# Optimization experiments

Measured on AMD Instinct MI355X. Metric: run time of the kernel, lower is better.

## Reference

```python
import jax, jax.numpy as jnp
import numpy as np

DIM = 1024
HID = 2732  # int(2*4*1024/3) rounded up to multiple of 4
E = 8
TOPK = 2
B, S = 2, 2048


def setup_inputs() -> dict:
    key = jax.random.key(0)
    ks = jax.random.split(key, 5)
    scale = 0.02
    return {
        "x": jax.random.normal(ks[0], (B, S, DIM), dtype=jnp.float32),
        "Wg": jax.random.normal(ks[1], (E, DIM), dtype=jnp.float32) * scale,
        "W1": jax.random.normal(ks[2], (E, HID, DIM), dtype=jnp.float32) * scale,
        "W2": jax.random.normal(ks[3], (E, DIM, HID), dtype=jnp.float32) * scale,
        "W3": jax.random.normal(ks[4], (E, HID, DIM), dtype=jnp.float32) * scale,
    }


def reference(x, Wg, W1, W2, W3):
    b, s, d = x.shape
    xt = x.reshape(b * s, d)                              # [N, d]
    scores = xt @ Wg.T                                    # [N, E]
    w, idx = jax.lax.top_k(scores, TOPK)                  # [N, k]
    w = jax.nn.softmax(w, axis=-1)
    n = xt.shape[0]
    # combine weights scattered back into [N, E] (top-k indices are distinct per row)
    cw = jnp.zeros((n, E), dtype=x.dtype).at[jnp.arange(n)[:, None], idx].set(w)
    # dense per-expert SwiGLU (mathematically identical to masked dispatch)
    h1 = jnp.einsum('nd,ehd->neh', xt, W1)                # [N, E, H]
    h3 = jnp.einsum('nd,ehd->neh', xt, W3)
    h = jax.nn.silu(h1) * h3
    y = jnp.einsum('neh,edh->ned', h, W2)                 # [N, E, d]
    out = jnp.einsum('ned,ne->nd', y, cw)                 # [N, d]
    return out
```

## Files before the change

### kernel.cpp

```cpp
#include <hip/hip_runtime.h>
#include <hip/hip_bf16.h>
#include <stdint.h>

#define DIM   1024
#define HID   2732
#define HPAD  2816
#define NEXP  8
#define NTOK  4096
#define NROW  8192
#define C13BLK 22528

typedef __attribute__((ext_vector_type(8))) short bf16x8;
typedef __attribute__((ext_vector_type(4))) float f32x4;

__device__ __forceinline__ unsigned short f2bf(float f) {
    union { float f; uint32_t u; } v; v.f = f;
    uint32_t u = v.u;
    return (unsigned short)((u + 0x7FFFu + ((u >> 16) & 1u)) >> 16);
}
__device__ __forceinline__ float bf2f(unsigned short h) {
    union { uint32_t u; float f; } v; v.u = ((uint32_t)h) << 16;
    return v.f;
}

#define ASYNC_CP16(g, l) __builtin_amdgcn_global_load_lds( \
    (const __attribute__((address_space(1))) void*)(g), \
    (__attribute__((address_space(3))) void*)(l), 16, 0, 0)

__device__ __forceinline__ void conv13_body(const float* __restrict__ src,
                                            unsigned short* __restrict__ dst, int blk) {
    size_t t = (size_t)blk * 256 + threadIdx.x;
    int d4 = (int)(t & 255);
    size_t rest = t >> 8;
    int hp = (int)(rest % HPAD);
    int e  = (int)(rest / HPAD);
    ushort4 o;
    if (hp < HID) {
        float4 v = *(const float4*)(src + ((size_t)e * HID + hp) * DIM + d4 * 4);
        o.x = f2bf(v.x); o.y = f2bf(v.y); o.z = f2bf(v.z); o.w = f2bf(v.w);
    } else {
        o.x = o.y = o.z = o.w = 0;
    }
    *(ushort4*)(dst + t * 4) = o;
}

__global__ void prep_kernel(const float* __restrict__ x,  const float* __restrict__ Wg,
                            const float* __restrict__ W1, const float* __restrict__ W2,
                            const float* __restrict__ W3,
                            unsigned short* __restrict__ W1b,
                            unsigned short* __restrict__ W2b,
                            unsigned short* __restrict__ W3b,
                            int* __restrict__ counts, int* __restrict__ a_exp,
                            int* __restrict__ a_rank, float* __restrict__ a_w) {
    int b = blockIdx.x;
    if (b < C13BLK) { conv13_body(W1, W1b, b); return; }
    b -= C13BLK;
    if (b < C13BLK) { conv13_body(W3, W3b, b); return; }
    b -= C13BLK;
    if (b < C13BLK) {
        size_t t = (size_t)b * 256 + threadIdx.x;
        int h4 = (int)(t % (HPAD / 4));
        size_t rest = t / (HPAD / 4);
        int d = (int)(rest % DIM);
        int e = (int)(rest / DIM);
        ushort4 o;
        if (h4 * 4 < HID) {
            float4 v = *(const float4*)(W2 + ((size_t)e * DIM + d) * HID + h4 * 4);
            o.x = f2bf(v.x); o.y = f2bf(v.y); o.z = f2bf(v.z); o.w = f2bf(v.w);
        } else {
            o.x = o.y = o.z = o.w = 0;
        }
        *(ushort4*)(W2b + t * 4) = o;
        return;
    }
    b -= C13BLK;
    int wave = threadIdx.x >> 6, lane = threadIdx.x & 63;
    int n = b * 4 + wave;
    const float* xr = x + (size_t)n * DIM + lane * 16;
    float p[NEXP];
#pragma unroll
    for (int e = 0; e < NEXP; ++e) p[e] = 0.f;
#pragma unroll
    for (int i = 0; i < 4; ++i) {
        float4 xv = *(const float4*)(xr + i * 4);
#pragma unroll
        for (int e = 0; e < NEXP; ++e) {
            float4 wv = *(const float4*)(Wg + e * DIM + lane * 16 + i * 4);
            p[e] += xv.x * wv.x + xv.y * wv.y + xv.z * wv.z + xv.w * wv.w;
        }
    }
#pragma unroll
    for (int off = 32; off > 0; off >>= 1)
#pragma unroll
        for (int e = 0; e < NEXP; ++e) p[e] += __shfl_xor(p[e], off);
    if (lane == 0) {
        int i1 = -1, i2 = -1; float m1 = -1e30f, m2 = -1e30f;
#pragma unroll
        for (int e = 0; e < NEXP; ++e) {
            float s = p[e];
            if (s > m1) { m2 = m1; i2 = i1; m1 = s; i1 = e; }
            else if (s > m2) { m2 = s; i2 = e; }
        }
        float e2 = __expf(m2 - m1);
        float inv = 1.f / (1.f + e2);
        int a = n * 2;
        a_exp[a] = i1;  a_w[a] = inv;        a_rank[a] = atomicAdd(&counts[i1], 1);
        a_exp[a+1] = i2; a_w[a+1] = e2 * inv; a_rank[a+1] = atomicAdd(&counts[i2], 1);
    }
}

__global__ void gather_kernel(const float* __restrict__ x, const int* __restrict__ a_exp,
                              const int* __restrict__ a_rank,
                              const int* __restrict__ counts,
                              unsigned short* __restrict__ XG,
                              int* __restrict__ row_of_a) {
    __shared__ int soff[NEXP];
    if (threadIdx.x == 0) {
        int s = 0;
#pragma unroll
        for (int e = 0; e < NEXP; ++e) { soff[e] = s; s += counts[e]; }
    }
    __syncthreads();
    int a = blockIdx.x, n = a >> 1;
    int row = soff[a_exp[a]] + a_rank[a];
    if (threadIdx.x == 0) row_of_a[a] = row;
    float4 xv = *(const float4*)(x + (size_t)n * DIM + threadIdx.x * 4);
    ushort4 o; o.x = f2bf(xv.x); o.y = f2bf(xv.y); o.z = f2bf(xv.z); o.w = f2bf(xv.w);
    *(ushort4*)(XG + (size_t)row * DIM + threadIdx.x * 4) = o;
}

__global__ __launch_bounds__(256, 2) void gemm1_kernel(
    const unsigned short* __restrict__ XG,
    const unsigned short* __restrict__ W1b,
    const unsigned short* __restrict__ W3b,
    const int* __restrict__ counts,
    unsigned short* __restrict__ Hbuf)
{
    const int e = blockIdx.z, mtile = blockIdx.y, ntile = blockIdx.x;
    const int cnt = counts[e];
    if (mtile * 128 >= cnt) return;
    int rowstart = 0;
    for (int i = 0; i < e; ++i) rowstart += counts[i];
    rowstart += mtile * 128;

    __shared__ __align__(16) unsigned short As[128 * 64];
    __shared__ __align__(16) unsigned short B1s[64 * 64];
    __shared__ __align__(16) unsigned short B3s[64 * 64];

    const int tid = threadIdx.x, lane = tid & 63, wave = tid >> 6;
    const int wm = wave >> 1, wn = wave & 1;
    const int quad = lane >> 4;

    const unsigned short* w1e = W1b + (size_t)e * HPAD * DIM;
    const unsigned short* w3e = W3b + (size_t)e * HPAD * DIM;

    const int srow = tid >> 3;
    const int scol = (((tid & 7) ^ (srow & 7)) * 8);
    const unsigned short* ag[4];
#pragma unroll
    for (int r = 0; r < 4; ++r) {
        int grow = rowstart + r * 32 + srow;
        if (grow > NROW - 1) grow = NROW - 1;
        ag[r] = XG + (size_t)grow * DIM + scol;
    }
    const unsigned short* bg1[2]; const unsigned short* bg3[2];
#pragma unroll
    for (int r = 0; r < 2; ++r) {
        int grow = ntile * 64 + r * 32 + srow;
        bg1[r] = w1e + (size_t)grow * DIM + scol;
        bg3[r] = w3e + (size_t)grow * DIM + scol;
    }

    f32x4 acc1[4][2], acc3[4][2];
#pragma unroll
    for (int i = 0; i < 4; ++i)
#pragma unroll
        for (int j = 0; j < 2; ++j) {
            acc1[i][j] = (f32x4){0.f, 0.f, 0.f, 0.f};
            acc3[i][j] = (f32x4){0.f, 0.f, 0.f, 0.f};
        }

    for (int kk = 0; kk < DIM / 64; ++kk) {
        const int k0 = kk * 64;
#pragma unroll
        for (int r = 0; r < 4; ++r)
            ASYNC_CP16(ag[r] + k0, &As[r * 2048 + tid * 8]);
#pragma unroll
        for (int r = 0; r < 2; ++r) {
            ASYNC_CP16(bg1[r] + k0, &B1s[r * 2048 + tid * 8]);
            ASYNC_CP16(bg3[r] + k0, &B3s[r * 2048 + tid * 8]);
        }
        __syncthreads();
#pragma unroll
        for (int ks = 0; ks < 2; ++ks) {
            const int cbase = ks * 4 + quad;
            bf16x8 af[4], b1f[2], b3f[2];
#pragma unroll
            for (int i = 0; i < 4; ++i) {
                int rl = wm * 64 + i * 16 + (lane & 15);
                af[i] = *(const bf16x8*)&As[rl * 64 + ((cbase ^ (rl & 7)) * 8)];
            }
#pragma unroll
            for (int j = 0; j < 2; ++j) {
                int rl1 = wn * 32 + j * 16 + (lane & 15);
                b1f[j] = *(const bf16x8*)&B1s[rl1 * 64 + ((cbase ^ (rl1 & 7)) * 8)];
                b3f[j] = *(const bf16x8*)&B3s[rl1 * 64 + ((cbase ^ (rl1 & 7)) * 8)];
            }
#pragma unroll
            for (int i = 0; i < 4; ++i)
#pragma unroll
                for (int j = 0; j < 2; ++j) {
                    acc1[i][j] = __builtin_amdgcn_mfma_f32_16x16x32_bf16(af[i], b1f[j], acc1[i][j], 0, 0, 0);
                    acc3[i][j] = __builtin_amdgcn_mfma_f32_16x16x32_bf16(af[i], b3f[j], acc3[i][j], 0, 0, 0);
                }
        }
        __syncthreads();
    }

    int mvalid = cnt - mtile * 128; if (mvalid > 128) mvalid = 128;
#pragma unroll
    for (int i = 0; i < 4; ++i)
#pragma unroll
        for (int r = 0; r < 4; ++r) {
            int rl = wm * 64 + i * 16 + quad * 4 + r;
            if (rl < mvalid) {
                size_t rowg = (size_t)(rowstart + rl);
#pragma unroll
                for (int j = 0; j < 2; ++j) {
                    float v1 = acc1[i][j][r], v3 = acc3[i][j][r];
                    float s = v1 / (1.f + __expf(-v1));
                    Hbuf[rowg * HPAD + ntile * 64 + wn * 32 + j * 16 + (lane & 15)] = f2bf(s * v3);
                }
            }
        }
}

__global__ __launch_bounds__(256, 2) void gemm2_kernel(
    const unsigned short* __restrict__ Hbuf,
    const unsigned short* __restrict__ W2b,
    const int* __restrict__ counts,
    unsigned short* __restrict__ Ybuf)
{
    const int e = blockIdx.z, mtile = blockIdx.y, ntile = blockIdx.x;
    const int cnt = counts[e];
    if (mtile * 128 >= cnt) return;
    int rowstart = 0;
    for (int i = 0; i < e; ++i) rowstart += counts[i];
    rowstart += mtile * 128;

    __shared__ __align__(16) unsigned short As[128 * 64];
    __shared__ __align__(16) unsigned short Bs[128 * 64];

    const int tid = threadIdx.x, lane = tid & 63, wave = tid >> 6;
    const int wm = wave >> 1, wn = wave & 1;
    const int quad = lane >> 4;

    const unsigned short* w2e = W2b + (size_t)e * DIM * HPAD;
    const int srow = tid >> 3;
    const int scol = (((tid & 7) ^ (srow & 7)) * 8);
    const unsigned short* ag[4]; const unsigned short* bg[4];
#pragma unroll
    for (int r = 0; r < 4; ++r) {
        int grow = rowstart + r * 32 + srow;
        if (grow > NROW - 1) grow = NROW - 1;
        ag[r] = Hbuf + (size_t)grow * HPAD + scol;
        bg[r] = w2e + (size_t)(ntile * 128 + r * 32 + srow) * HPAD + scol;
    }

    f32x4 acc[4][4];
#pragma unroll
    for (int i = 0; i < 4; ++i)
#pragma unroll
        for (int j = 0; j < 4; ++j) acc[i][j] = (f32x4){0.f, 0.f, 0.f, 0.f};

    for (int kk = 0; kk < HPAD / 64; ++kk) {
        const int k0 = kk * 64;
#pragma unroll
        for (int r = 0; r < 4; ++r) {
            ASYNC_CP16(ag[r] + k0, &As[r * 2048 + tid * 8]);
            ASYNC_CP16(bg[r] + k0, &Bs[r * 2048 + tid * 8]);
        }
        __syncthreads();
#pragma unroll
        for (int ks = 0; ks < 2; ++ks) {
            const int cbase = ks * 4 + quad;
            bf16x8 af[4], bf[4];
#pragma unroll
            for (int i = 0; i < 4; ++i) {
                int rla = wm * 64 + i * 16 + (lane & 15);
                int rlb = wn * 64 + i * 16 + (lane & 15);
                af[i] = *(const bf16x8*)&As[rla * 64 + ((cbase ^ (rla & 7)) * 8)];
                bf[i] = *(const bf16x8*)&Bs[rlb * 64 + ((cbase ^ (rlb & 7)) * 8)];
            }
#pragma unroll
            for (int i = 0; i < 4; ++i)
#pragma unroll
                for (int j = 0; j < 4; ++j)
                    acc[i][j] = __builtin_amdgcn_mfma_f32_16x16x32_bf16(af[i], bf[j], acc[i][j], 0, 0, 0);
        }
        __syncthreads();
    }

    int mvalid = cnt - mtile * 128; if (mvalid > 128) mvalid = 128;
#pragma unroll
    for (int i = 0; i < 4; ++i)
#pragma unroll
        for (int r = 0; r < 4; ++r) {
            int rl = wm * 64 + i * 16 + quad * 4 + r;
            if (rl < mvalid) {
                int rowg = rowstart + rl;
                unsigned short* yrow = Ybuf + (size_t)rowg * DIM + ntile * 128 + wn * 64 + (lane & 15);
#pragma unroll
                for (int j = 0; j < 4; ++j)
                    yrow[j * 16] = f2bf(acc[i][j][r]);
            }
        }
}

__global__ void combine_kernel(const unsigned short* __restrict__ Ybuf,
                               const int* __restrict__ row_of_a,
                               const float* __restrict__ a_w,
                               float* __restrict__ out) {
    int n = blockIdx.x, t = threadIdx.x;
    int r0 = row_of_a[2 * n], r1 = row_of_a[2 * n + 1];
    float w0 = a_w[2 * n], w1 = a_w[2 * n + 1];
    ushort4 y0 = *(const ushort4*)(Ybuf + (size_t)r0 * DIM + t * 4);
    ushort4 y1 = *(const ushort4*)(Ybuf + (size_t)r1 * DIM + t * 4);
    float4 o;
    o.x = w0 * bf2f(y0.x) + w1 * bf2f(y1.x);
    o.y = w0 * bf2f(y0.y) + w1 * bf2f(y1.y);
    o.z = w0 * bf2f(y0.z) + w1 * bf2f(y1.z);
    o.w = w0 * bf2f(y0.w) + w1 * bf2f(y1.w);
    *(float4*)(out + (size_t)n * DIM + t * 4) = o;
}

extern "C" void kernel_launch(void* const* d_in, const int* in_sizes, int n_in,
                              void* d_out, int out_size, void* d_ws, size_t ws_size,
                              hipStream_t stream) {
    const float* x  = (const float*)d_in[0];
    const float* Wg = (const float*)d_in[1];
    const float* W1 = (const float*)d_in[2];
    const float* W2 = (const float*)d_in[3];
    const float* W3 = (const float*)d_in[4];
    float* out = (float*)d_out;

    char* ws = (char*)d_ws;
    size_t off = 0;
    auto alloc = [&](size_t bytes) -> void* {
        void* p = ws + off;
        off = (off + bytes + 255) & ~(size_t)255;
        return p;
    };
    int*   counts      = (int*)alloc(NEXP * 4);
    int*   a_exp       = (int*)alloc(NROW * 4);
    int*   a_rank      = (int*)alloc(NROW * 4);
    float* a_w         = (float*)alloc(NROW * 4);
    int*   row_of_a    = (int*)alloc(NROW * 4);
    unsigned short* XG   = (unsigned short*)alloc((size_t)NROW * DIM * 2);
    unsigned short* Hbuf = (unsigned short*)alloc((size_t)NROW * HPAD * 2);
    unsigned short* W1b  = (unsigned short*)alloc((size_t)NEXP * HPAD * DIM * 2);
    unsigned short* W3b  = (unsigned short*)alloc((size_t)NEXP * HPAD * DIM * 2);
    unsigned short* W2b  = (unsigned short*)alloc((size_t)NEXP * DIM * HPAD * 2);
    unsigned short* Ybuf = (unsigned short*)W1b;

    hipMemsetAsync(counts, 0, NEXP * 4, stream);

    prep_kernel<<<3 * C13BLK + NTOK / 4, 256, 0, stream>>>(
        x, Wg, W1, W2, W3, W1b, W2b, W3b, counts, a_exp, a_rank, a_w);
    gather_kernel<<<NROW, 256, 0, stream>>>(x, a_exp, a_rank, counts, XG, row_of_a);

    gemm1_kernel<<<dim3(HPAD / 64, 64, NEXP), 256, 0, stream>>>(
        XG, W1b, W3b, counts, Hbuf);
    gemm2_kernel<<<dim3(DIM / 128, 64, NEXP), 256, 0, stream>>>(
        Hbuf, W2b, counts, Ybuf);
    combine_kernel<<<NTOK, 256, 0, stream>>>(Ybuf, row_of_a, a_w, out);
}
```

Measured before the change: 575.9 us.

## Shrink hidden padding, use grid-stride weight conversion, split W2 conversion into own kernel

Result: slower. 622.4 us (+8.1%).

```diff
diff --git a/kernel.cpp b/kernel.cpp
--- a/kernel.cpp
+++ b/kernel.cpp
@@ -4,11 +4,17 @@
 
 #define DIM   1024
 #define HID   2732
-#define HPAD  2816
+#define HPAD  2752
 #define NEXP  8
 #define NTOK  4096
 #define NROW  8192
-#define C13BLK 22528
+
+#define G13   (NEXP * HPAD * (DIM / 4))
+#define GALL  (2 * G13)
+#define G2    (NEXP * DIM * (HPAD / 4))
+#define CONV13_BLKS 2048
+#define CONV2_BLKS  1024
+#define ROUTE_BLKS  (NTOK / 4)
 
 typedef __attribute__((ext_vector_type(8))) short bf16x8;
 typedef __attribute__((ext_vector_type(4))) float f32x4;
@@ -27,53 +33,49 @@
     (const __attribute__((address_space(1))) void*)(g), \
     (__attribute__((address_space(3))) void*)(l), 16, 0, 0)
 
-__device__ __forceinline__ void conv13_body(const float* __restrict__ src,
-                                            unsigned short* __restrict__ dst, int blk) {
-    size_t t = (size_t)blk * 256 + threadIdx.x;
-    int d4 = (int)(t & 255);
-    size_t rest = t >> 8;
-    int hp = (int)(rest % HPAD);
-    int e  = (int)(rest / HPAD);
-    ushort4 o;
-    if (hp < HID) {
-        float4 v = *(const float4*)(src + ((size_t)e * HID + hp) * DIM + d4 * 4);
-        o.x = f2bf(v.x); o.y = f2bf(v.y); o.z = f2bf(v.z); o.w = f2bf(v.w);
-    } else {
-        o.x = o.y = o.z = o.w = 0;
-    }
-    *(ushort4*)(dst + t * 4) = o;
-}
-
-__global__ void prep_kernel(const float* __restrict__ x,  const float* __restrict__ Wg,
-                            const float* __restrict__ W1, const float* __restrict__ W2,
-                            const float* __restrict__ W3,
-                            unsigned short* __restrict__ W1b,
-                            unsigned short* __restrict__ W2b,
-                            unsigned short* __restrict__ W3b,
-                            int* __restrict__ counts, int* __restrict__ a_exp,
-                            int* __restrict__ a_rank, float* __restrict__ a_w) {
+__global__ void prep1_kernel(const float* __restrict__ x,  const float* __restrict__ Wg,
+                             const float* __restrict__ W1, const float* __restrict__ W3,
+                             unsigned short* __restrict__ W1b,
+                             unsigned short* __restrict__ W3b,
+                             int* __restrict__ counts, int* __restrict__ a_exp,
+                             int* __restrict__ a_rank, float* __restrict__ a_w) {
     int b = blockIdx.x;
-    if (b < C13BLK) { conv13_body(W1, W1b, b); return; }
-    b -= C13BLK;
-    if (b < C13BLK) { conv13_body(W3, W3b, b); return; }
-    b -= C13BLK;
-    if (b < C13BLK) {
-        size_t t = (size_t)b * 256 + threadIdx.x;
-        int h4 = (int)(t % (HPAD / 4));
-        size_t rest = t / (HPAD / 4);
-        int d = (int)(rest % DIM);
-        int e = (int)(rest / DIM);
-        ushort4 o;
-        if (h4 * 4 < HID) {
-            float4 v = *(const float4*)(W2 + ((size_t)e * DIM + d) * HID + h4 * 4);
-            o.x = f2bf(v.x); o.y = f2bf(v.y); o.z = f2bf(v.z); o.w = f2bf(v.w);
-        } else {
-            o.x = o.y = o.z = o.w = 0;
-        }
-        *(ushort4*)(W2b + t * 4) = o;
+    if (b < CONV13_BLKS) {
+        const uint32_t nthr = CONV13_BLKS * 256;
+        uint32_t t0 = (uint32_t)b * 256 + threadIdx.x;
+        for (uint32_t g0 = t0; g0 < (uint32_t)GALL; g0 += nthr * 4) {
+            float4 v[4]; uint32_t gs[4]; bool ok[4];
+#pragma unroll
+            for (int k = 0; k < 4; ++k) {
+                uint32_t g = g0 + (uint32_t)k * nthr;
+                gs[k] = g; ok[k] = g < (uint32_t)GALL;
+                v[k] = (float4){0.f, 0.f, 0.f, 0.f};
+                if (ok[k]) {
+                    uint32_t gg = g < (uint32_t)G13 ? g : g - (uint32_t)G13;
+                    const float* src = g < (uint32_t)G13 ? W1 : W3;
+                    uint32_t d4 = gg & 255;
+                    uint32_t rest = gg >> 8;
+                    uint32_t hp = rest % HPAD;
+                    uint32_t e  = rest / HPAD;
+                    if (hp < HID)
+                        v[k] = *(const float4*)(src + ((size_t)e * HID + hp) * DIM + d4 * 4);
+                }
+            }
+#pragma unroll
+            for (int k = 0; k < 4; ++k) {
+                if (ok[k]) {
+                    unsigned short* dst = gs[k] < (uint32_t)G13 ? W1b : W3b;
+                    uint32_t gg = gs[k] < (uint32_t)G13 ? gs[k] : gs[k] - (uint32_t)G13;
+                    ushort4 o;
+                    o.x = f2bf(v[k].x); o.y = f2bf(v[k].y);
+                    o.z = f2bf(v[k].z); o.w = f2bf(v[k].w);
+                    *(ushort4*)(dst + (size_t)gg * 4) = o;
+                }
+            }
+        }
         return;
     }
-    b -= C13BLK;
+    b -= CONV13_BLKS;
     int wave = threadIdx.x >> 6, lane = threadIdx.x & 63;
     int n = b * 4 + wave;
     const float* xr = x + (size_t)n * DIM + lane * 16;
@@ -106,6 +108,38 @@
         int a = n * 2;
         a_exp[a] = i1;  a_w[a] = inv;        a_rank[a] = atomicAdd(&counts[i1], 1);
         a_exp[a+1] = i2; a_w[a+1] = e2 * inv; a_rank[a+1] = atomicAdd(&counts[i2], 1);
+    }
+}
+
+__global__ void conv2_kernel(const float* __restrict__ W2,
+                             unsigned short* __restrict__ W2b) {
+    const uint32_t nthr = CONV2_BLKS * 256;
+    uint32_t t0 = (uint32_t)blockIdx.x * 256 + threadIdx.x;
+    for (uint32_t g0 = t0; g0 < (uint32_t)G2; g0 += nthr * 4) {
+        float4 v[4]; uint32_t gs[4]; bool ok[4];
+#pragma unroll
+        for (int k = 0; k < 4; ++k) {
+            uint32_t g = g0 + (uint32_t)k * nthr;
+            gs[k] = g; ok[k] = g < (uint32_t)G2;
+            v[k] = (float4){0.f, 0.f, 0.f, 0.f};
+            if (ok[k]) {
+                uint32_t h4 = g % (HPAD / 4);
+                uint32_t rest = g / (HPAD / 4);
+                uint32_t d = rest & (DIM - 1);
+                uint32_t e = rest >> 10;
+                if (h4 * 4 < HID)
+                    v[k] = *(const float4*)(W2 + ((size_t)e * DIM + d) * HID + h4 * 4);
+            }
+        }
+#pragma unroll
+        for (int k = 0; k < 4; ++k) {
+            if (ok[k]) {
+                ushort4 o;
+                o.x = f2bf(v[k].x); o.y = f2bf(v[k].y);
+                o.z = f2bf(v[k].z); o.w = f2bf(v[k].w);
+                *(ushort4*)(W2b + (size_t)gs[k] * 4) = o;
+            }
+        }
     }
 }
 
@@ -365,12 +399,13 @@
 
     hipMemsetAsync(counts, 0, NEXP * 4, stream);
 
-    prep_kernel<<<3 * C13BLK + NTOK / 4, 256, 0, stream>>>(
-        x, Wg, W1, W2, W3, W1b, W2b, W3b, counts, a_exp, a_rank, a_w);
+    prep1_kernel<<<CONV13_BLKS + ROUTE_BLKS, 256, 0, stream>>>(
+        x, Wg, W1, W3, W1b, W3b, counts, a_exp, a_rank, a_w);
     gather_kernel<<<NROW, 256, 0, stream>>>(x, a_exp, a_rank, counts, XG, row_of_a);
 
     gemm1_kernel<<<dim3(HPAD / 64, 64, NEXP), 256, 0, stream>>>(
         XG, W1b, W3b, counts, Hbuf);
+    conv2_kernel<<<CONV2_BLKS, 256, 0, stream>>>(W2, W2b);
     gemm2_kernel<<<dim3(DIM / 128, 64, NEXP), 256, 0, stream>>>(
         Hbuf, W2b, counts, Ybuf);
     combine_kernel<<<NTOK, 256, 0, stream>>>(Ybuf, row_of_a, a_w, out);
```
